# Performance work log

Hardware: AMD Instinct MI355X
Metric: run time of the kernel (lower is better)

## Reference

```python
import jax, jax.numpy as jnp
import numpy as np

HID = 256
NL = 4
NC = 5
SPACE = 16


def _grid_sample(feat, grid):
    # feat [B,C,H,W]; grid [B,Hg,Wg,2] in [-1,1]; bilinear, align_corners=True, zeros padding
    B, C, H, W = feat.shape
    x = (grid[..., 0] + 1.0) * 0.5 * (W - 1)
    y = (grid[..., 1] + 1.0) * 0.5 * (H - 1)
    x0f = jnp.floor(x)
    y0f = jnp.floor(y)
    wx1 = x - x0f
    wy1 = y - y0f

    def corner(yf, xf, wgt):
        valid = (xf >= 0) & (xf <= W - 1) & (yf >= 0) & (yf <= H - 1)
        xi = jnp.clip(xf, 0, W - 1).astype(jnp.int32)
        yi = jnp.clip(yf, 0, H - 1).astype(jnp.int32)
        v = jax.vmap(lambda f, yy, xx: f[:, yy, xx])(feat, yi, xi)  # [B,C,Hg,Wg]
        return v * (wgt * valid.astype(feat.dtype))[:, None]

    return (corner(y0f, x0f, (1 - wy1) * (1 - wx1))
            + corner(y0f, x0f + 1, (1 - wy1) * wx1)
            + corner(y0f + 1, x0f, wy1 * (1 - wx1))
            + corner(y0f + 1, x0f + 1, wy1 * wx1))


def _conv(x, w, b, pad):
    y = jax.lax.conv_general_dilated(x, w, (1, 1), ((pad, pad), (pad, pad)),
                                     dimension_numbers=('NCHW', 'OIHW', 'NCHW'))
    return y + b[None, :, None, None]


def _resize_ac(x, oh, ow):
    # bilinear resize with align_corners=True
    B, C, H, W = x.shape
    ys = jnp.linspace(0.0, H - 1.0, oh)
    xs = jnp.linspace(0.0, W - 1.0, ow)
    y0 = jnp.floor(ys).astype(jnp.int32)
    y1 = jnp.minimum(y0 + 1, H - 1)
    x0 = jnp.floor(xs).astype(jnp.int32)
    x1 = jnp.minimum(x0 + 1, W - 1)
    wy = (ys - y0)[None, None, :, None]
    wx = (xs - x0)[None, None, None, :]
    top = x[:, :, y0, :] * (1 - wy) + x[:, :, y1, :] * wy
    return top[:, :, :, x0] * (1 - wx) + top[:, :, :, x1] * wx


def _mlp(x, w1, b1, w2, b2):
    # 2-layer MLP, dropout is identity at inference
    return jax.nn.relu(x @ w1 + b1) @ w2 + b2


def setup_inputs() -> dict:
    key = jax.random.key(0)
    ks = jax.random.split(key, 16)
    B, H, W = 8, 512, 512

    def rn(k, shape, s=0.02):
        return jax.random.normal(k, shape, jnp.float32) * s

    return {
        'images': jax.random.normal(ks[0], (B, 3, H, W), jnp.float32),
        'feat0': jax.random.normal(ks[1], (B, HID, 128, 128), jnp.float32),
        'feat1': jax.random.normal(ks[2], (B, HID, 64, 64), jnp.float32),
        'feat2': jax.random.normal(ks[3], (B, HID, 32, 32), jnp.float32),
        'feat3': jax.random.normal(ks[4], (B, HID, 16, 16), jnp.float32),
        'mask_feat': jax.random.normal(ks[5], (B, HID, 128, 128), jnp.float32),
        'o': jax.random.normal(ks[6], (B, 16, 16, 768), jnp.float32),
        'dw1': rn(ks[7], (768, HID)), 'db1': jnp.zeros((HID,), jnp.float32),
        'dw2': rn(ks[8], (HID, 8)), 'db2': jnp.zeros((8,), jnp.float32),
        'cw1': rn(ks[9], (HID, HID)), 'cb1': jnp.zeros((HID,), jnp.float32),
        'cw2': rn(ks[10], (HID, NC + 1)), 'cb2': jnp.zeros((NC + 1,), jnp.float32),
        'conv_w': rn(ks[11], (HID, HID * NL, 3, 3)), 'conv_b': jnp.zeros((HID,), jnp.float32),
        'mw1': rn(ks[12], (HID, HID, 3, 3)), 'mb1': jnp.zeros((HID,), jnp.float32),
        'bn_g': jnp.ones((HID,), jnp.float32), 'bn_b': jnp.zeros((HID,), jnp.float32),
        'bn_m': jnp.zeros((HID,), jnp.float32), 'bn_v': jnp.ones((HID,), jnp.float32),
        'mw2': rn(ks[13], (1, HID, 1, 1)), 'mb2': jnp.zeros((1,), jnp.float32),
    }


def reference(images, feat0, feat1, feat2, feat3, mask_feat, o,
              dw1, db1, dw2, db2, cw1, cb1, cw2, cb2, conv_w, conv_b,
              mw1, mb1, bn_g, bn_b, bn_m, bn_v, mw2, mb2):
    B, _, H, W = images.shape
    ny = int(np.ceil(H / SPACE))
    nx = int(np.ceil(W / SPACE))
    # AnchorPoints: meshgrid 'xy', scaled by space, shifted by half-cell origin
    gx, gy = jnp.meshgrid(jnp.arange(nx, dtype=jnp.float32), jnp.arange(ny, dtype=jnp.float32))
    origin = jnp.array([(W % SPACE) or SPACE, (H % SPACE) or SPACE], jnp.float32) / 2
    anchors = jnp.stack([gx, gy], -1) * SPACE + origin  # [ny,nx,2] (x,y)

    # learned offsets: MLP then pixel-shuffle style 16x16x8 -> 32x32x2
    d = _mlp(o, dw1, db1, dw2, db2)  # [B,16,16,8]
    d = d.reshape(B, 16, 16, 2, 2, 2).transpose(0, 1, 3, 2, 4, 5).reshape(B, 32, 32, 2)
    prop = anchors[None] + d  # deformed proposals [B,32,32,2]

    feats = [feat0, feat1, feat2, feat3]
    strides = [4, 8, 16, 32]
    rois = []
    for f, s in zip(feats, strides):
        fh, fw = f.shape[2], f.shape[3]
        grid = 2.0 * prop / s / jnp.array([fw, fh], jnp.float32) - 1.0
        rois.append(_grid_sample(f, grid))
    roi = jnp.concatenate(rois, 1)  # [B, HID*NL, 32, 32]
    roi = _conv(roi, conv_w, conv_b, 1).transpose(0, 2, 3, 1)  # [B,32,32,HID]
    logits = _mlp(roi, cw1, cb1, cw2, cb2)  # [B,32,32,NC+1]

    # mask head: conv3x3 -> BN(eval) -> ReLU -> conv1x1(pad=1) -> bilinear upsample (align_corners=True)
    m = _conv(mask_feat, mw1, mb1, 1)
    m = m * (bn_g * jax.lax.rsqrt(bn_v + 1e-5))[None, :, None, None] \
        + (bn_b - bn_m * bn_g * jax.lax.rsqrt(bn_v + 1e-5))[None, :, None, None]
    m = jax.nn.relu(m)
    m = _conv(m, mw2, mb2, 1)  # 1x1 conv with padding=1 -> [B,1,130,130] (as in source)
    masks = _resize_ac(m, H, W)  # [B,1,H,W]

    return (prop.reshape(B, -1, 2), logits.reshape(B, -1, NC + 1), masks)
```

## Files before the change

### kernel.cpp

```cpp
#include <hip/hip_runtime.h>
#include <hip/hip_bf16.h>
#include <cstdint>
#include <cstddef>

using bf16x8 = __attribute__((ext_vector_type(8))) short;
using f32x4  = __attribute__((ext_vector_type(4))) float;

static constexpr size_t PART_OFF = 4194308;
static constexpr size_t WT_OFF   = 16777220;
static constexpr size_t WTR_SH   = (size_t)294912 * 8;
static constexpr size_t WTM_SH   = (size_t)73728 * 8;
static constexpr size_t M2P_OFF  = WT_OFF + (WTR_SH + WTM_SH) / 2;

__device__ __forceinline__ uint32_t pk2(float a, float b) {
  __hip_bfloat162 h = __float22bfloat162_rn(make_float2(a, b));
  union { __hip_bfloat162 h; uint32_t u; } c; c.h = h;
  return c.u;
}

__device__ __forceinline__ void gld16(const void* g, void* l) {
  __builtin_amdgcn_global_load_lds(
      (const __attribute__((address_space(1))) void*)g,
      (__attribute__((address_space(3))) void*)l, 16, 0, 0);
}

#define CBAR(N) do { \
    asm volatile("s_waitcnt vmcnt(" #N ")" ::: "memory"); \
    __builtin_amdgcn_sched_barrier(0); \
    __builtin_amdgcn_s_barrier(); \
    __builtin_amdgcn_sched_barrier(0); } while (0)

__global__ __launch_bounds__(256) void k_prep_w(
    const float* __restrict__ conv_w, const float* __restrict__ mw1,
    short* __restrict__ wTr, short* __restrict__ wTm, float* __restrict__ zp) {
  __shared__ float sm[16 * 292];
  int t = threadIdx.x;
  int bid = blockIdx.x;
  if (bid == 0 && t < 4) zp[t] = 0.f;
  bool is_m = (bid >= 512);
  int b2 = is_m ? (bid - 512) : bid;
  int kidx = is_m ? (b2 & 7) : (b2 & 31);
  int cog  = is_m ? (b2 >> 3) : (b2 >> 5);
  const float* src = is_m ? mw1 : conv_w;
  short* dst = is_m ? wTm : wTr;
  int CI = is_m ? 256 : 1024;
  int ci0 = kidx * 32;
  int co0 = cog * 16;
  for (int e = t; e < 4608; e += 256) {
    int row = e / 288, pos = e - row * 288;
    sm[row * 292 + pos] = src[((size_t)(co0 + row) * CI + ci0) * 9 + pos];
  }
  __syncthreads();
  int nb = cog >> 3, cofrag = cog & 7;
  for (int e = t; e < 576; e += 256) {
    int tap = e >> 6, kg = (e >> 4) & 3, lr = e & 15;
    float v[8];
#pragma unroll
    for (int j = 0; j < 8; ++j) v[j] = sm[lr * 292 + (kg * 8 + j) * 9 + tap];
    uint4 pk = make_uint4(pk2(v[0], v[1]), pk2(v[2], v[3]),
                          pk2(v[4], v[5]), pk2(v[6], v[7]));
    size_t chunk = ((size_t)(kidx * 2 + nb) * 9 + tap) * 512
                 + cofrag * 64 + kg * 16 + lr;
    *(uint4*)&dst[chunk * 8] = pk;
  }
}

__global__ __launch_bounds__(256) void k_prop(
    const float* __restrict__ o,
    const float* __restrict__ dw1, const float* __restrict__ db1,
    const float* __restrict__ dw2, const float* __restrict__ db2,
    float* __restrict__ prop) {
  __shared__ float o_lds[4 * 768];
  __shared__ float h_lds[4 * 256];
  int t = threadIdx.x;
  int bid = blockIdx.x;
  int b = bid >> 6;
  int rem = bid & 63;
  int i = rem >> 2;
  int j0 = (rem & 3) * 4;
  const float* obase = o + ((size_t)(b * 16 + i) * 16 + j0) * 768;
  for (int e = t; e < 4 * 768; e += 256) o_lds[e] = obase[e];
  __syncthreads();
  float h0 = 0.f, h1 = 0.f, h2 = 0.f, h3 = 0.f;
  for (int k = 0; k < 768; ++k) {
    float w = dw1[k * 256 + t];
    h0 = fmaf(o_lds[k], w, h0);
    h1 = fmaf(o_lds[768 + k], w, h1);
    h2 = fmaf(o_lds[1536 + k], w, h2);
    h3 = fmaf(o_lds[2304 + k], w, h3);
  }
  float bb = db1[t];
  h_lds[t]        = fmaxf(h0 + bb, 0.f);
  h_lds[256 + t]  = fmaxf(h1 + bb, 0.f);
  h_lds[512 + t]  = fmaxf(h2 + bb, 0.f);
  h_lds[768 + t]  = fmaxf(h3 + bb, 0.f);
  __syncthreads();
  if (t < 32) {
    int pos = t >> 3;
    int c   = t & 7;
    float acc = db2[c];
    const float* hp = h_lds + pos * 256;
    for (int k = 0; k < 256; ++k) acc = fmaf(hp[k], dw2[k * 8 + c], acc);
    int p = c >> 2, q = (c >> 1) & 1, cc = c & 1;
    int row = 2 * i + p;
    int col = 2 * (j0 + pos) + q;
    float anchor = (cc == 0) ? ((float)col * 16.f + 8.f) : ((float)row * 16.f + 8.f);
    prop[((size_t)(b * 32 + row) * 32 + col) * 2 + cc] = anchor + acc;
  }
}

__global__ __launch_bounds__(256) void k_sample(
    const float* __restrict__ f0, const float* __restrict__ f1,
    const float* __restrict__ f2, const float* __restrict__ f3,
    const float* __restrict__ prop, uint4* __restrict__ bfR) {
  int py = blockIdx.x;
  int l  = blockIdx.y;
  int b  = blockIdx.z;
  int t  = threadIdx.x;
  int xq = t & 31;
  int cq = t >> 5;
  const float* f = (l == 0) ? f0 : (l == 1) ? f1 : (l == 2) ? f2 : f3;
  int fsz = 128 >> l;
  float s = (float)(4 << l);

  size_t pidx = ((size_t)b * 32 + py) * 32 + xq;
  float px = prop[pidx * 2 + 0];
  float pv = prop[pidx * 2 + 1];
  float gx = 2.f * px / s / (float)fsz - 1.f;
  float gy = 2.f * pv / s / (float)fsz - 1.f;
  float x = (gx + 1.f) * 0.5f * (float)(fsz - 1);
  float y = (gy + 1.f) * 0.5f * (float)(fsz - 1);
  float x0f = floorf(x), y0f = floorf(y);
  float wx1 = x - x0f, wy1 = y - y0f;

  int off[4];
  float wgt[4];
#pragma unroll
  for (int cy = 0; cy < 2; ++cy) {
#pragma unroll
    for (int cx = 0; cx < 2; ++cx) {
      float xf = x0f + (float)cx;
      float yf = y0f + (float)cy;
      float w = (cy ? wy1 : (1.f - wy1)) * (cx ? wx1 : (1.f - wx1));
      bool valid = (xf >= 0.f) && (xf <= (float)(fsz - 1)) &&
                   (yf >= 0.f) && (yf <= (float)(fsz - 1));
      int xi = (int)fminf(fmaxf(xf, 0.f), (float)(fsz - 1));
      int yi = (int)fminf(fmaxf(yf, 0.f), (float)(fsz - 1));
      off[cy * 2 + cx] = yi * fsz + xi;
      wgt[cy * 2 + cx] = valid ? w : 0.f;
    }
  }
  const float* fb = f + (size_t)b * 256 * fsz * fsz;
#pragma unroll
  for (int i = 0; i < 4; ++i) {
    int cgl = i * 8 + cq;
    float v[8];
#pragma unroll
    for (int j = 0; j < 8; ++j) {
      const float* fc = fb + (size_t)(cgl * 8 + j) * fsz * fsz;
      v[j] = wgt[0] * fc[off[0]] + wgt[1] * fc[off[1]] +
             wgt[2] * fc[off[2]] + wgt[3] * fc[off[3]];
    }
    bfR[(((size_t)b * 128 + l * 32 + cgl) * 32 + py) * 32 + xq] =
        make_uint4(pk2(v[0], v[1]), pk2(v[2], v[3]),
                   pk2(v[4], v[5]), pk2(v[6], v[7]));
  }
}

__global__ __launch_bounds__(256) void k_cvt(const float* __restrict__ mf,
                                             uint4* __restrict__ bfA) {
  int d = blockIdx.x * 256 + threadIdx.x;
  int x = d & 127, y = (d >> 7) & 127, cg = (d >> 14) & 31, b = d >> 19;
  const float* src = mf + (((size_t)(b * 256 + cg * 8)) << 14) + (y << 7) + x;
  float v[8];
#pragma unroll
  for (int j = 0; j < 8; ++j) v[j] = src[(size_t)j << 14];
  bfA[d] = make_uint4(pk2(v[0], v[1]), pk2(v[2], v[3]),
                      pk2(v[4], v[5]), pk2(v[6], v[7]));
}

__global__ __launch_bounds__(512, 2) void k_roi_mfma(
    const uint4* __restrict__ bfR, const short* __restrict__ wTr,
    float* __restrict__ part) {
  __shared__ __align__(16) short A_s[2][1408 * 8];
  __shared__ __align__(16) short B_s[4608 * 8];
  int t = threadIdx.x;
  int lane = t & 63, wv = t >> 6, wm = wv >> 1, wn = wv & 1;
  int kg = lane >> 4, lr = lane & 15;
  int bid = blockIdx.x;
  int nb = bid & 1;
  int mi = (bid >> 1) & 31;
  int b = mi >> 2, yt = mi & 3;
  int ks = bid >> 6;

  f32x4 acc[4][4];
#pragma unroll
  for (int m = 0; m < 4; ++m)
#pragma unroll
    for (int n = 0; n < 4; ++n) acc[m][n] = {0.f, 0.f, 0.f, 0.f};

  const uint4* aptr[3];
  int astep[3], aldst[3];
  bool aon[3];
#pragma unroll
  for (int i = 0; i < 3; ++i) {
    int wq = wv + 8 * i;
    aon[i] = wq < 22;
    int c = wq * 64 + lane;
    int pxi = c >> 2, slot = c & 3;
    int r = pxi / 34;
    int x = pxi - r * 34 - 1;
    int y = yt * 8 + r - 1;
    int cg4 = slot ^ ((pxi >> 1) & 3);
    bool ok = (r < 10) && (x >= 0) && (x < 32) && (y >= 0) && (y < 32);
    long chunk = ok ? (long)((((b * 128 + ks * 32 + cg4) * 32 + y) * 32) + x) : -1L;
    aptr[i] = bfR + chunk;
    astep[i] = ok ? 4096 : 0;
    aldst[i] = wq * 512;
  }
  int bg1[5], bl1[5], bg2[4], bl2[4];
#pragma unroll
  for (int j = 0; j < 5; ++j) {
    int w = wv + 8 * j;
    bg1[j] = (w * 64 + lane) * 8;
    bl1[j] = w * 512;
  }
#pragma unroll
  for (int j = 0; j < 4; ++j) {
    int w = wv + 8 * j;
    bg2[j] = (2560 + w * 64 + lane) * 8;
    bl2[j] = 20480 + w * 512;
  }
  const size_t BKC = (size_t)4608 * 8;
  const short* bbase = wTr + ((size_t)(ks * 8) * 2 + nb) * BKC;

#define ROI_ISSUE_A(BUF)                                         \
  {                                                              \
    _Pragma("unroll")                                            \
    for (int i = 0; i < 3; ++i)                                  \
      if (aon[i]) {                                              \
        gld16(aptr[i], &A_s[BUF][aldst[i]]);                     \
        aptr[i] += astep[i];                                     \
      }                                                          \
  }
#define ROI_ISSUE_H1(KC)                                         \
  {                                                              \
    const short* bk = bbase + (size_t)(KC) * 2 * BKC;            \
    _Pragma("unroll")                                            \
    for (int j = 0; j < 5; ++j) gld16(bk + bg1[j], &B_s[bl1[j]]);\
  }
#define ROI_ISSUE_H2(KC)                                         \
  {                                                              \
    const short* bk = bbase + (size_t)(KC) * 2 * BKC;            \
    _Pragma("unroll")                                            \
    for (int j = 0; j < 4; ++j) gld16(bk + bg2[j], &B_s[bl2[j]]);\
  }

#define ROI_TAPS(T0, T1)                                                          \
  {                                                                               \
    _Pragma("unroll")                                                             \
    for (int tap = (T0); tap < (T1); ++tap) {                                     \
      int ky = tap / 3, kx = tap - ky * 3;                                        \
      bf16x8 bfr[4];                                                              \
      _Pragma("unroll")                                                           \
      for (int n = 0; n < 4; ++n)                                                 \
        bfr[n] = *(const bf16x8*)&B_s[((((tap * 8 + wn * 4 + n) * 4 + kg) * 16)   \
                                       + lr) * 8];                                \
      _Pragma("unroll")                                                           \
      for (int m = 0; m < 4; ++m) {                                               \
        int pb = wm * 64 + m * 16;                                                \
        int px = ((pb >> 5) + ky) * 34 + (pb & 31) + lr + kx;                     \
        bf16x8 af = *(const bf16x8*)&As[(px * 4 + ((kg ^ (px >> 1)) & 3)) * 8];   \
        _Pragma("unroll")                                                         \
        for (int n = 0; n < 4; ++n)                                               \
          acc[m][n] = __builtin_amdgcn_mfma_f32_16x16x32_bf16(af, bfr[n],         \
                                                              acc[m][n], 0, 0, 0);\
      }                                                                           \
    }                                                                             \
  }

  ROI_ISSUE_H1(0);
  ROI_ISSUE_A(0);
  __syncthreads();

  for (int kc = 0; kc < 7; ++kc) {
    int buf = kc & 1;
    const short* As = A_s[buf];
    ROI_ISSUE_H2(kc);
    ROI_ISSUE_A(buf ^ 1);
    __builtin_amdgcn_s_setprio(1);
    ROI_TAPS(0, 5);
    __builtin_amdgcn_s_setprio(0);
    CBAR(2);
    ROI_ISSUE_H1(kc + 1);
    __builtin_amdgcn_s_setprio(1);
    ROI_TAPS(5, 9);
    __builtin_amdgcn_s_setprio(0);
    CBAR(0);
  }
  {
    const short* As = A_s[1];
    ROI_ISSUE_H2(7);
    __builtin_amdgcn_s_setprio(1);
    ROI_TAPS(0, 5);
    __builtin_amdgcn_s_setprio(0);
    CBAR(0);
    __builtin_amdgcn_s_setprio(1);
    ROI_TAPS(5, 9);
    __builtin_amdgcn_s_setprio(0);
  }
#pragma unroll
  for (int m = 0; m < 4; ++m)
#pragma unroll
    for (int r = 0; r < 4; ++r) {
      int p = wm * 64 + m * 16 + kg * 4 + r;
      int y = yt * 8 + (p >> 5), x = p & 31;
      float* dst = part + (size_t)ks * 2097152 + (((size_t)b * 32 + y) * 32 + x) * 256
                        + nb * 128 + wn * 64 + lr;
#pragma unroll
      for (int n = 0; n < 4; ++n) dst[n * 16] = acc[m][n][r];
    }
}

__global__ __launch_bounds__(256) void k_mlp(
    const float* __restrict__ part, const float* __restrict__ conv_b,
    const float* __restrict__ cw1, const float* __restrict__ cb1,
    const float* __restrict__ cw2, const float* __restrict__ cb2,
    float* __restrict__ logits) {
  __shared__ float v[1024];
  __shared__ float h[1024];
  int t = threadIdx.x;
  size_t base = (size_t)blockIdx.x * 1024;
  const size_t CH = (size_t)8192 * 256;
  for (int e = t; e < 1024; e += 256) {
    float s = part[base + e] + part[CH + base + e] +
              part[2 * CH + base + e] + part[3 * CH + base + e];
    v[e] = s + conv_b[e & 255];
  }
  __syncthreads();
  float a0 = cb1[t], a1 = a0, a2 = a0, a3 = a0;
  for (int k = 0; k < 256; ++k) {
    float w = cw1[k * 256 + t];
    a0 = fmaf(v[k], w, a0);
    a1 = fmaf(v[256 + k], w, a1);
    a2 = fmaf(v[512 + k], w, a2);
    a3 = fmaf(v[768 + k], w, a3);
  }
  h[t]       = fmaxf(a0, 0.f);
  h[256 + t] = fmaxf(a1, 0.f);
  h[512 + t] = fmaxf(a2, 0.f);
  h[768 + t] = fmaxf(a3, 0.f);
  __syncthreads();
  if (t < 24) {
    int pos = t / 6, c = t - 6 * pos;
    float acc = cb2[c];
    const float* hp = h + pos * 256;
    for (int k = 0; k < 256; ++k) acc = fmaf(hp[k], cw2[k * 6 + c], acc);
    logits[((size_t)blockIdx.x * 4 + pos) * 6 + c] = acc;
  }
}

__global__ __launch_bounds__(512, 2) void k_mask_mfma(
    const uint4* __restrict__ bfA, const short* __restrict__ wTm,
    const float* __restrict__ mb1,
    const float* __restrict__ bn_g, const float* __restrict__ bn_b,
    const float* __restrict__ bn_m, const float* __restrict__ bn_v,
    const float* __restrict__ mw2, float* __restrict__ m2p) {
  __shared__ __align__(16) short A_s[2][2112 * 8];
  __shared__ __align__(16) short B_s[4608 * 8];
  int t = threadIdx.x;
  int lane = t & 63, wv = t >> 6, wm = wv >> 1, wn = wv & 1;
  int kg = lane >> 4, lr = lane & 15;
  int bid = blockIdx.x;
  int nb = bid & 1;
  int tile = bid >> 1;
  int b = tile >> 6, yt = tile & 63;

  f32x4 acc[4][4];
#pragma unroll
  for (int m = 0; m < 4; ++m)
#pragma unroll
    for (int n = 0; n < 4; ++n) acc[m][n] = {0.f, 0.f, 0.f, 0.f};

  const uint4* aptr[5];
  int astep[5], aldst[5];
  bool aon[5];
#pragma unroll
  for (int i = 0; i < 5; ++i) {
    int wq = wv + 8 * i;
    aon[i] = wq < 33;
    int c = wq * 64 + lane;
    int pxi = c >> 2, slot = c & 3;
    int r = pxi / 130;
    int x = pxi - r * 130 - 1;
    int y = 2 * yt + r - 1;
    int cg4 = slot ^ ((pxi >> 1) & 3);
    bool ok = (r < 4) && (x >= 0) && (x < 128) && (y >= 0) && (y < 128);
    long chunk = ok ? (long)((((b * 32 + cg4) * 128 + y) * 128) + x) : -1L;
    aptr[i] = bfA + chunk;
    astep[i] = ok ? 65536 : 0;
    aldst[i] = wq * 512;
  }
  int bg1[5], bl1[5], bg2[4], bl2[4];
#pragma unroll
  for (int j = 0; j < 5; ++j) {
    int w = wv + 8 * j;
    bg1[j] = (w * 64 + lane) * 8;
    bl1[j] = w * 512;
  }
#pragma unroll
  for (int j = 0; j < 4; ++j) {
    int w = wv + 8 * j;
    bg2[j] = (2560 + w * 64 + lane) * 8;
    bl2[j] = 20480 + w * 512;
  }
  const size_t BKC = (size_t)4608 * 8;
  const short* bbase = wTm + (size_t)nb * BKC;

#define MSK_ISSUE_A(BUF)                                         \
  {                                                              \
    _Pragma("unroll")                                            \
    for (int i = 0; i < 5; ++i)                                  \
      if (aon[i]) {                                              \
        gld16(aptr[i], &A_s[BUF][aldst[i]]);                     \
        aptr[i] += astep[i];                                     \
      }                                                          \
  }
#define MSK_ISSUE_H1(KC)                                         \
  {                                                              \
    const short* bk = bbase + (size_t)(KC) * 2 * BKC;            \
    _Pragma("unroll")                                            \
    for (int j = 0; j < 5; ++j) gld16(bk + bg1[j], &B_s[bl1[j]]);\
  }
#define MSK_ISSUE_H2(KC)                                         \
  {                                                              \
    const short* bk = bbase + (size_t)(KC) * 2 * BKC;            \
    _Pragma("unroll")                                            \
    for (int j = 0; j < 4; ++j) gld16(bk + bg2[j], &B_s[bl2[j]]);\
  }

#define MSK_TAPS(T0, T1)                                                          \
  {                                                                               \
    _Pragma("unroll")                                                             \
    for (int tap = (T0); tap < (T1); ++tap) {                                     \
      int ky = tap / 3, kx = tap - ky * 3;                                        \
      bf16x8 bfr[4];                                                              \
      _Pragma("unroll")                                                           \
      for (int n = 0; n < 4; ++n)                                                 \
        bfr[n] = *(const bf16x8*)&B_s[((((tap * 8 + wn * 4 + n) * 4 + kg) * 16)   \
                                       + lr) * 8];                                \
      _Pragma("unroll")                                                           \
      for (int m = 0; m < 4; ++m) {                                               \
        int px = ((wm >> 1) + ky) * 130 + (wm & 1) * 64 + m * 16 + lr + kx;       \
        bf16x8 af = *(const bf16x8*)&As[(px * 4 + ((kg ^ (px >> 1)) & 3)) * 8];   \
        _Pragma("unroll")                                                         \
        for (int n = 0; n < 4; ++n)                                               \
          acc[m][n] = __builtin_amdgcn_mfma_f32_16x16x32_bf16(af, bfr[n],         \
                                                              acc[m][n], 0, 0, 0);\
      }                                                                           \
    }                                                                             \
  }

  MSK_ISSUE_H1(0);
  MSK_ISSUE_A(0);
  __syncthreads();

  for (int kc = 0; kc < 7; ++kc) {
    int buf = kc & 1;
    const short* As = A_s[buf];
    MSK_ISSUE_H2(kc);
    MSK_ISSUE_A(buf ^ 1);
    __builtin_amdgcn_s_setprio(1);
    MSK_TAPS(0, 5);
    __builtin_amdgcn_s_setprio(0);
    CBAR(4);
    MSK_ISSUE_H1(kc + 1);
    __builtin_amdgcn_s_setprio(1);
    MSK_TAPS(5, 9);
    __builtin_amdgcn_s_setprio(0);
    CBAR(0);
  }
  {
    const short* As = A_s[1];
    MSK_ISSUE_H2(7);
    __builtin_amdgcn_s_setprio(1);
    MSK_TAPS(0, 5);
    __builtin_amdgcn_s_setprio(0);
    CBAR(0);
    __builtin_amdgcn_s_setprio(1);
    MSK_TAPS(5, 9);
    __builtin_amdgcn_s_setprio(0);
  }

  float sc[4], sh[4], w2v[4], b1[4];
#pragma unroll
  for (int n = 0; n < 4; ++n) {
    int co = nb * 128 + wn * 64 + n * 16 + lr;
    float s = bn_g[co] * rsqrtf(bn_v[co] + 1e-5f);
    sc[n] = s;
    sh[n] = bn_b[co] - bn_m[co] * s;
    b1[n] = mb1[co];
    w2v[n] = mw2[co];
  }
  float* red = (float*)&A_s[0][0];
#pragma unroll
  for (int m = 0; m < 4; ++m)
#pragma unroll
    for (int r = 0; r < 4; ++r) {
      int p = (wm >> 1) * 128 + (wm & 1) * 64 + m * 16 + kg * 4 + r;
      float s = 0.f;
#pragma unroll
      for (int n = 0; n < 4; ++n) {
        float z = fmaf(acc[m][n][r] + b1[n], sc[n], sh[n]);
        s = fmaf(w2v[n], fmaxf(z, 0.f), s);
      }
      red[p * 32 + wn * 16 + lr] = s;
    }
  __syncthreads();
  if (t < 256) {
    float s = 0.f;
#pragma unroll
    for (int q = 0; q < 32; ++q) s += red[t * 32 + q];
    int y = 2 * yt + (t >> 7);
    int x = t & 127;
    m2p[(size_t)nb * 131072 + ((size_t)b * 128 + y) * 128 + x] = s;
  }
}

__global__ __launch_bounds__(256) void k_resize(const float* __restrict__ m2p,
                                                const float* __restrict__ mb2,
                                                float* __restrict__ masks) {
  int idx = blockIdx.x * 256 + threadIdx.x;
  int b = idx >> 18;
  int rem = idx & 262143;
  int y = rem >> 9;
  int x = rem & 511;
  const float SC = 129.0f / 511.0f;
  float sy = (float)y * SC;
  float sx = (float)x * SC;
  float y0f = floorf(sy), x0f = floorf(sx);
  int y0 = (int)y0f, x0 = (int)x0f;
  int y1 = min(y0 + 1, 129), x1 = min(x0 + 1, 129);
  float wy = sy - y0f, wx = sx - x0f;
  float base = mb2[0];
  const float* p0 = m2p + (size_t)b * 16384;
  const float* p1 = m2p + 131072 + (size_t)b * 16384;

  auto corner = [&](int yy, int xx) -> float {
    if (yy >= 1 && yy <= 128 && xx >= 1 && xx <= 128) {
      int o2 = (yy - 1) * 128 + (xx - 1);
      return base + p0[o2] + p1[o2];
    }
    return base;
  };
  float tv = corner(y0, x0) * (1.f - wx) + corner(y0, x1) * wx;
  float bv = corner(y1, x0) * (1.f - wx) + corner(y1, x1) * wx;
  masks[idx] = tv * (1.f - wy) + bv * wy;
}

extern "C" void kernel_launch(void* const* d_in, const int* in_sizes, int n_in,
                              void* d_out, int out_size, void* d_ws, size_t ws_size,
                              hipStream_t stream) {
  (void)in_sizes; (void)n_in; (void)out_size; (void)ws_size;
  const float* f0        = (const float*)d_in[1];
  const float* f1        = (const float*)d_in[2];
  const float* f2        = (const float*)d_in[3];
  const float* f3        = (const float*)d_in[4];
  const float* mask_feat = (const float*)d_in[5];
  const float* o         = (const float*)d_in[6];
  const float* dw1       = (const float*)d_in[7];
  const float* db1       = (const float*)d_in[8];
  const float* dw2       = (const float*)d_in[9];
  const float* db2       = (const float*)d_in[10];
  const float* cw1       = (const float*)d_in[11];
  const float* cb1       = (const float*)d_in[12];
  const float* cw2       = (const float*)d_in[13];
  const float* cb2       = (const float*)d_in[14];
  const float* conv_w    = (const float*)d_in[15];
  const float* conv_b    = (const float*)d_in[16];
  const float* mw1       = (const float*)d_in[17];
  const float* mb1       = (const float*)d_in[18];
  const float* bn_g      = (const float*)d_in[19];
  const float* bn_b      = (const float*)d_in[20];
  const float* bn_m      = (const float*)d_in[21];
  const float* bn_v      = (const float*)d_in[22];
  const float* mw2       = (const float*)d_in[23];
  const float* mb2       = (const float*)d_in[24];

  float* ws   = (float*)d_ws;
  uint4* bf   = (uint4*)(ws + 4);
  float* part = ws + PART_OFF;
  short* wTr  = (short*)(ws + WT_OFF);
  short* wTm  = wTr + WTR_SH;
  float* m2p  = ws + M2P_OFF;

  float* out_prop   = (float*)d_out;
  float* out_logits = out_prop + (size_t)8 * 1024 * 2;
  float* out_masks  = out_logits + (size_t)8 * 1024 * 6;

  hipLaunchKernelGGL(k_prep_w, dim3(640), dim3(256), 0, stream,
                     conv_w, mw1, wTr, wTm, ws);
  hipLaunchKernelGGL(k_prop, dim3(512), dim3(256), 0, stream,
                     o, dw1, db1, dw2, db2, out_prop);
  hipLaunchKernelGGL(k_sample, dim3(32, 4, 8), dim3(256), 0, stream,
                     f0, f1, f2, f3, out_prop, bf);
  hipLaunchKernelGGL(k_roi_mfma, dim3(256), dim3(512), 0, stream,
                     bf, wTr, part);
  hipLaunchKernelGGL(k_mlp, dim3(2048), dim3(256), 0, stream,
                     part, conv_b, cw1, cb1, cw2, cb2, out_logits);
  hipLaunchKernelGGL(k_cvt, dim3(16384), dim3(256), 0, stream,
                     mask_feat, bf);
  hipLaunchKernelGGL(k_mask_mfma, dim3(1024), dim3(512), 0, stream,
                     bf, wTm, mb1, bn_g, bn_b, bn_m, bn_v, mw2, m2p);
  hipLaunchKernelGGL(k_resize, dim3(8192), dim3(256), 0, stream,
                     m2p, mb2, out_masks);
}
```

Baseline: 350.8 us.

## Enlarge mask conv tile to 8x64 pixels per block with doubled accumulators

The 3x3 mask conv kernel moves from 2-row x 128-column output tiles to 8-row x 64-column tiles, so each block computes 512 pixels instead of 256. Each wave now holds 8x4 MFMA accumulators, and the grid is halved to 512 blocks. The taller tile cuts halo overhead per output (10 input rows for 8 output rows instead of 4 for 2), and each weight fragment is reused across twice as many pixels. The reduction buffer gets a stride of 33 to avoid LDS bank conflicts. In exchange it uses more registers and LDS per block, which may reduce occupancy, and the smaller grid may fill the CUs less evenly.

```diff
diff --git a/kernel.cpp b/kernel.cpp
--- a/kernel.cpp
+++ b/kernel.cpp
@@ -366,7 +366,7 @@
     const float* __restrict__ bn_g, const float* __restrict__ bn_b,
     const float* __restrict__ bn_m, const float* __restrict__ bn_v,
     const float* __restrict__ mw2, float* __restrict__ m2p) {
-  __shared__ __align__(16) short A_s[2][2112 * 8];
+  __shared__ __align__(16) short A_s[2][2640 * 8];
   __shared__ __align__(16) short B_s[4608 * 8];
   int t = threadIdx.x;
   int lane = t & 63, wv = t >> 6, wm = wv >> 1, wn = wv & 1;
@@ -374,32 +374,38 @@
   int bid = blockIdx.x;
   int nb = bid & 1;
   int tile = bid >> 1;
-  int b = tile >> 6, yt = tile & 63;
-
-  f32x4 acc[4][4];
-#pragma unroll
-  for (int m = 0; m < 4; ++m)
+  int b = tile >> 5;
+  int ti = tile & 31;
+  int rt = ti >> 1;
+  int ct = ti & 1;
+
+  f32x4 acc[8][4];
+#pragma unroll
+  for (int m = 0; m < 8; ++m)
 #pragma unroll
     for (int n = 0; n < 4; ++n) acc[m][n] = {0.f, 0.f, 0.f, 0.f};
 
-  const uint4* aptr[5];
-  int astep[5], aldst[5];
-  bool aon[5];
-#pragma unroll
-  for (int i = 0; i < 5; ++i) {
+  const uint4* aptr[6];
+  int astep[6], aldst[6];
+  bool aon[6];
+#pragma unroll
+  for (int i = 0; i < 6; ++i) {
     int wq = wv + 8 * i;
-    aon[i] = wq < 33;
     int c = wq * 64 + lane;
-    int pxi = c >> 2, slot = c & 3;
-    int r = pxi / 130;
-    int x = pxi - r * 130 - 1;
-    int y = 2 * yt + r - 1;
+    bool on = c < 2640;
+    int cc = on ? c : 0;
+    int pxi = cc >> 2, slot = cc & 3;
+    int rr = pxi / 66;
+    int xx = pxi - rr * 66;
+    int y = rt * 8 + rr - 1;
+    int x = ct * 64 + xx - 1;
     int cg4 = slot ^ ((pxi >> 1) & 3);
-    bool ok = (r < 4) && (x >= 0) && (x < 128) && (y >= 0) && (y < 128);
+    bool ok = on && (y >= 0) && (y < 128) && (x >= 0) && (x < 128);
     long chunk = ok ? (long)((((b * 32 + cg4) * 128 + y) * 128) + x) : -1L;
     aptr[i] = bfA + chunk;
     astep[i] = ok ? 65536 : 0;
     aldst[i] = wq * 512;
+    aon[i] = on;
   }
   int bg1[5], bl1[5], bg2[4], bl2[4];
 #pragma unroll
@@ -420,7 +426,7 @@
 #define MSK_ISSUE_A(BUF)                                         \
   {                                                              \
     _Pragma("unroll")                                            \
-    for (int i = 0; i < 5; ++i)                                  \
+    for (int i = 0; i < 6; ++i)                                  \
       if (aon[i]) {                                              \
         gld16(aptr[i], &A_s[BUF][aldst[i]]);                     \
         aptr[i] += astep[i];                                     \
@@ -450,9 +456,9 @@
         bfr[n] = *(const bf16x8*)&B_s[((((tap * 8 + wn * 4 + n) * 4 + kg) * 16)   \
                                        + lr) * 8];                                \
       _Pragma("unroll")                                                           \
-      for (int m = 0; m < 4; ++m) {                                               \
-        int px = ((wm >> 1) + ky) * 130 + (wm & 1) * 64 + m * 16 + lr + kx;       \
-        bf16x8 af = *(const bf16x8*)&As[(px * 4 + ((kg ^ (px >> 1)) & 3)) * 8];   \
+      for (int m = 0; m < 8; ++m) {                                               \
+        int pxi = (2 * wm + (m >> 2) + ky) * 66 + (m & 3) * 16 + lr + kx;         \
+        bf16x8 af = *(const bf16x8*)&As[(pxi * 4 + ((kg ^ (pxi >> 1)) & 3)) * 8]; \
         _Pragma("unroll")                                                         \
         for (int n = 0; n < 4; ++n)                                               \
           acc[m][n] = __builtin_amdgcn_mfma_f32_16x16x32_bf16(af, bfr[n],         \
@@ -473,7 +479,7 @@
     __builtin_amdgcn_s_setprio(1);
     MSK_TAPS(0, 5);
     __builtin_amdgcn_s_setprio(0);
-    CBAR(4);
+    CBAR(5);
     MSK_ISSUE_H1(kc + 1);
     __builtin_amdgcn_s_setprio(1);
     MSK_TAPS(5, 9);
@@ -502,27 +508,28 @@
     b1[n] = mb1[co];
     w2v[n] = mw2[co];
   }
+  __syncthreads();
   float* red = (float*)&A_s[0][0];
 #pragma unroll
-  for (int m = 0; m < 4; ++m)
+  for (int m = 0; m < 8; ++m)
 #pragma unroll
     for (int r = 0; r < 4; ++r) {
-      int p = (wm >> 1) * 128 + (wm & 1) * 64 + m * 16 + kg * 4 + r;
+      int p = wm * 128 + m * 16 + kg * 4 + r;
       float s = 0.f;
 #pragma unroll
       for (int n = 0; n < 4; ++n) {
         float z = fmaf(acc[m][n][r] + b1[n], sc[n], sh[n]);
         s = fmaf(w2v[n], fmaxf(z, 0.f), s);
       }
-      red[p * 32 + wn * 16 + lr] = s;
+      red[p * 33 + wn * 16 + lr] = s;
     }
   __syncthreads();
-  if (t < 256) {
+  {
     float s = 0.f;
 #pragma unroll
-    for (int q = 0; q < 32; ++q) s += red[t * 32 + q];
-    int y = 2 * yt + (t >> 7);
-    int x = t & 127;
+    for (int q = 0; q < 32; ++q) s += red[t * 33 + q];
+    int y = rt * 8 + (t >> 6);
+    int x = ct * 64 + (t & 63);
     m2p[(size_t)nb * 131072 + ((size_t)b * 128 + y) * 128 + x] = s;
   }
 }
@@ -610,7 +617,7 @@
                      part, conv_b, cw1, cb1, cw2, cb2, out_logits);
   hipLaunchKernelGGL(k_cvt, dim3(16384), dim3(256), 0, stream,
                      mask_feat, bf);
-  hipLaunchKernelGGL(k_mask_mfma, dim3(1024), dim3(512), 0, stream,
+  hipLaunchKernelGGL(k_mask_mfma, dim3(512), dim3(512), 0, stream,
                      bf, wTm, mb1, bn_g, bn_b, bn_m, bn_v, mw2, m2p);
   hipLaunchKernelGGL(k_resize, dim3(8192), dim3(256), 0, stream,
                      m2p, mb2, out_masks);
```

After: 630.6 us. 79.8% more time.
